# Kernel optimization log

Measured on AMD Instinct MI355X. Metric: run time of the kernel, lower is better.

Reference implementation:

```python
import jax, jax.numpy as jnp
import numpy as np

N_NODES = 50000
N_EDGES = 800000
D = 128


def setup_inputs() -> dict:
    key = jax.random.key(0)
    ks = jax.random.split(key, 7)
    stdv = 1.0 / np.sqrt(D)
    inputs = jax.random.normal(ks[0], (N_NODES, D), dtype=jnp.float32)
    weight = jax.random.uniform(ks[1], (D, D), dtype=jnp.float32, minval=-stdv, maxval=stdv)
    bias = jax.random.uniform(ks[2], (D,), dtype=jnp.float32, minval=-stdv, maxval=stdv)
    alpha = jax.random.uniform(ks[3], (2, 1, 1), dtype=jnp.float32, minval=-3.0, maxval=3.0)
    adj_vals = jax.random.uniform(ks[4], (N_EDGES,), dtype=jnp.float32)
    adj_rows = jax.random.randint(ks[5], (N_EDGES,), 0, N_NODES, dtype=jnp.int32)
    adj_cols = jax.random.randint(ks[6], (N_EDGES,), 0, N_NODES, dtype=jnp.int32)
    return {"inputs": inputs, "weight": weight, "bias": bias, "alpha": alpha,
            "adj_vals": adj_vals, "adj_rows": adj_rows, "adj_cols": adj_cols}


def reference(inputs, weight, bias, alpha, adj_vals, adj_rows, adj_cols):
    n = inputs.shape[0]
    # support = inputs @ weight  (dense GEMM; spmm with dense lhs == matmul)
    support = inputs @ weight                                  # [N, D]
    # output = adj @ support  as COO SpMM: gather source rows, scale, scatter-add
    gathered = support[adj_cols] * adj_vals[:, None]           # [E, D]
    agg = jax.ops.segment_sum(gathered, adj_rows, num_segments=n)  # [N, D]
    # softmax-gated combine of [agg, inputs] (stack order: output first)
    gate = jax.nn.softmax(alpha, axis=0)                       # [2,1,1]
    out = agg * gate[0] + inputs * gate[1]                     # [N, D]
    return jax.nn.elu(out + bias)
```

## Files before the change

kernel.cpp:

```cpp
#include <hip/hip_runtime.h>

#define N_NODES 50000
#define N_EDGES 800000
#define D 128

typedef __attribute__((ext_vector_type(8))) short bf16x8;
typedef __attribute__((ext_vector_type(4))) float f32x4;
typedef __attribute__((ext_vector_type(4))) short short4v;

__device__ __forceinline__ short f2bf(float f) {
    unsigned u = __float_as_uint(f);
    unsigned r = u + 0x7FFFu + ((u >> 16) & 1u);
    return (short)(r >> 16);
}
__device__ __forceinline__ float bf2f(short s) {
    return __uint_as_float(((unsigned)(unsigned short)s) << 16);
}

__global__ __launch_bounds__(256) void gemm_hist_kernel(
    const float* __restrict__ inp, const float* __restrict__ W,
    short* __restrict__ support, const int* __restrict__ rows,
    int* __restrict__ counts, int nGemmBlocks)
{
    if ((int)blockIdx.x >= nGemmBlocks) {
        int e = ((int)blockIdx.x - nGemmBlocks) * 256 + threadIdx.x;
        if (e < N_EDGES) atomicAdd(&counts[rows[e]], 1);
        return;
    }

    __shared__ short Wt[128][136];
    const int tid = threadIdx.x;

    #pragma unroll
    for (int i = 0; i < 16; ++i) {
        int lin = i * 1024 + tid * 4;
        int k = lin >> 7, c = lin & 127;
        float4 w = *(const float4*)&W[lin];
        Wt[c + 0][k] = f2bf(w.x);
        Wt[c + 1][k] = f2bf(w.y);
        Wt[c + 2][k] = f2bf(w.z);
        Wt[c + 3][k] = f2bf(w.w);
    }
    __syncthreads();

    const int wid = tid >> 6, lane = tid & 63;
    const int lr = lane & 15;
    const int lg = lane >> 4;
    const int m0 = (int)blockIdx.x * 64 + wid * 16;

    int arow = m0 + lr;
    if (arow >= N_NODES) arow = 0;
    const float* aptr = &inp[(size_t)arow * D + lg * 8];

    f32x4 acc[8] = {};
    #pragma unroll
    for (int kc = 0; kc < 4; ++kc) {
        float4 a0 = *(const float4*)(aptr + kc * 32);
        float4 a1 = *(const float4*)(aptr + kc * 32 + 4);
        bf16x8 af;
        af[0] = f2bf(a0.x); af[1] = f2bf(a0.y); af[2] = f2bf(a0.z); af[3] = f2bf(a0.w);
        af[4] = f2bf(a1.x); af[5] = f2bf(a1.y); af[6] = f2bf(a1.z); af[7] = f2bf(a1.w);
        #pragma unroll
        for (int t = 0; t < 8; ++t) {
            const bf16x8 bf = *(const bf16x8*)&Wt[t * 16 + lr][kc * 32 + lg * 8];
            acc[t] = __builtin_amdgcn_mfma_f32_16x16x32_bf16(af, bf, acc[t], 0, 0, 0);
        }
    }
    #pragma unroll
    for (int t = 0; t < 8; ++t) {
        #pragma unroll
        for (int r = 0; r < 4; ++r) {
            int orow = m0 + lg * 4 + r;
            if (orow < N_NODES)
                support[(size_t)orow * D + t * 16 + lr] = f2bf(acc[t][r]);
        }
    }
}

__global__ __launch_bounds__(256) void scan_fused(
    const int* __restrict__ counts, int* __restrict__ offsets,
    int* __restrict__ cursor, unsigned long long* __restrict__ aggFlag,
    int* __restrict__ ticket)
{
    __shared__ int s[256];
    __shared__ int bid_s, prefix_s;
    if (threadIdx.x == 0) bid_s = atomicAdd(ticket, 1);
    __syncthreads();
    const int bid = bid_s;
    const int gid = bid * 256 + threadIdx.x;
    int v = (gid < N_NODES) ? counts[gid] : 0;
    s[threadIdx.x] = v;
    __syncthreads();
    #pragma unroll
    for (int d = 1; d < 256; d <<= 1) {
        int t = (threadIdx.x >= d) ? s[threadIdx.x - d] : 0;
        __syncthreads();
        s[threadIdx.x] += t;
        __syncthreads();
    }
    if (threadIdx.x == 0) {
        unsigned long long pk = (1ULL << 63) | (unsigned long long)(unsigned)s[255];
        __hip_atomic_store(&aggFlag[bid], pk, __ATOMIC_RELAXED, __HIP_MEMORY_SCOPE_AGENT);
    }
    if (threadIdx.x < 64) {
        int sum = 0;
        for (int j = threadIdx.x; j < bid; j += 64) {
            unsigned long long pk;
            while (((pk = __hip_atomic_load(&aggFlag[j], __ATOMIC_RELAXED,
                                            __HIP_MEMORY_SCOPE_AGENT)) >> 63) == 0)
                __builtin_amdgcn_s_sleep(1);
            sum += (int)(unsigned)(pk & 0xFFFFFFFFULL);
        }
        #pragma unroll
        for (int d = 1; d < 64; d <<= 1) sum += __shfl_xor(sum, d);
        if (threadIdx.x == 0) prefix_s = sum;
    }
    __syncthreads();
    if (gid < N_NODES) {
        int o = prefix_s + s[threadIdx.x] - v;
        offsets[gid] = o;
        cursor[gid] = o;
    }
    if (gid == 0) offsets[N_NODES] = N_EDGES;
}

#define SCAT_GROUPS 8
#define SCAT_BPG    392
__global__ __launch_bounds__(256) void scatter_kernel(
    const int* __restrict__ rows, const int* __restrict__ cols,
    const float* __restrict__ vals, int* __restrict__ cursor,
    int2* __restrict__ pairs)
{
    const int g  = blockIdx.x & (SCAT_GROUPS - 1);
    const int gi = blockIdx.x >> 3;
    const int rowLo = g * (N_NODES / SCAT_GROUPS);
    const int rowHi = rowLo + (N_NODES / SCAT_GROUPS);

    for (int e = gi * 256 + threadIdx.x; e < N_EDGES; e += SCAT_BPG * 256) {
        int r = rows[e];
        if (r >= rowLo && r < rowHi) {
            int p = atomicAdd(&cursor[r], 1);
            int2 pk;
            pk.x = cols[e];
            pk.y = __float_as_int(vals[e]);
            pairs[p] = pk;
        }
    }
}

__global__ __launch_bounds__(256) void agg_fused(
    const short* __restrict__ support, const int* __restrict__ offsets,
    const int2* __restrict__ pairs,
    const float* __restrict__ inp, const float* __restrict__ bias,
    const float* __restrict__ alpha, float* __restrict__ out)
{
    const int wv = (blockIdx.x * 256 + threadIdx.x) >> 6;
    const int lane = threadIdx.x & 63;
    if (wv >= N_NODES) return;
    const int half = lane >> 5;
    const int li = lane & 31;

    const int start = offsets[wv];
    const int end   = offsets[wv + 1];

    const float4 x = *(const float4*)&inp[(size_t)wv * D + li * 4];
    const float4 b4 = *(const float4*)&bias[li * 4];
    const float a0 = alpha[0], a1 = alpha[1];

    float4 acc = make_float4(0.f, 0.f, 0.f, 0.f);
    int e = start;
    for (; e + 8 <= end; e += 8) {
        int2 p0 = pairs[e + 0 + half];
        int2 p1 = pairs[e + 2 + half];
        int2 p2 = pairs[e + 4 + half];
        int2 p3 = pairs[e + 6 + half];
        short4v s0 = *(const short4v*)&support[(size_t)p0.x * D + li * 4];
        short4v s1 = *(const short4v*)&support[(size_t)p1.x * D + li * 4];
        short4v s2 = *(const short4v*)&support[(size_t)p2.x * D + li * 4];
        short4v s3 = *(const short4v*)&support[(size_t)p3.x * D + li * 4];
        float v0 = __int_as_float(p0.y), v1 = __int_as_float(p1.y);
        float v2 = __int_as_float(p2.y), v3 = __int_as_float(p3.y);
        acc.x += v0 * bf2f(s0[0]) + v1 * bf2f(s1[0]) + v2 * bf2f(s2[0]) + v3 * bf2f(s3[0]);
        acc.y += v0 * bf2f(s0[1]) + v1 * bf2f(s1[1]) + v2 * bf2f(s2[1]) + v3 * bf2f(s3[1]);
        acc.z += v0 * bf2f(s0[2]) + v1 * bf2f(s1[2]) + v2 * bf2f(s2[2]) + v3 * bf2f(s3[2]);
        acc.w += v0 * bf2f(s0[3]) + v1 * bf2f(s1[3]) + v2 * bf2f(s2[3]) + v3 * bf2f(s3[3]);
    }
    for (; e < end; e += 2) {
        int idx = e + half;
        int2 p = (idx < end) ? pairs[idx] : make_int2(0, 0);
        float v = __int_as_float(p.y);
        short4v s = *(const short4v*)&support[(size_t)p.x * D + li * 4];
        acc.x += v * bf2f(s[0]);
        acc.y += v * bf2f(s[1]);
        acc.z += v * bf2f(s[2]);
        acc.w += v * bf2f(s[3]);
    }

    acc.x += __shfl_xor(acc.x, 32);
    acc.y += __shfl_xor(acc.y, 32);
    acc.z += __shfl_xor(acc.z, 32);
    acc.w += __shfl_xor(acc.w, 32);

    const float m = fmaxf(a0, a1);
    const float e0 = __expf(a0 - m), e1 = __expf(a1 - m);
    const float inv = 1.f / (e0 + e1);
    const float g0 = e0 * inv, g1 = e1 * inv;

    float t0 = acc.x * g0 + x.x * g1 + b4.x;
    float t1 = acc.y * g0 + x.y * g1 + b4.y;
    float t2 = acc.z * g0 + x.z * g1 + b4.z;
    float t3 = acc.w * g0 + x.w * g1 + b4.w;
    float r0 = t0 > 0.f ? t0 : (__expf(t0) - 1.f);
    float r1 = t1 > 0.f ? t1 : (__expf(t1) - 1.f);
    float r2 = t2 > 0.f ? t2 : (__expf(t2) - 1.f);
    float r3 = t3 > 0.f ? t3 : (__expf(t3) - 1.f);

    float2 o = (half == 0) ? make_float2(r0, r1) : make_float2(r2, r3);
    *(float2*)&out[(size_t)wv * D + li * 4 + half * 2] = o;
}

extern "C" void kernel_launch(void* const* d_in, const int* in_sizes, int n_in,
                              void* d_out, int out_size, void* d_ws, size_t ws_size,
                              hipStream_t stream)
{
    const float* inp   = (const float*)d_in[0];
    const float* W     = (const float*)d_in[1];
    const float* bias  = (const float*)d_in[2];
    const float* alpha = (const float*)d_in[3];
    const float* vals  = (const float*)d_in[4];
    const int*   rows  = (const int*)d_in[5];
    const int*   cols  = (const int*)d_in[6];
    float* out = (float*)d_out;

    short* support  = (short*)d_ws;
    int*   counts   = (int*)(support + (size_t)N_NODES * D);
    int*   ticket   = counts + N_NODES;
    unsigned long long* aggFlag = (unsigned long long*)(ticket + 2);
    int*   offsets  = (int*)(aggFlag + 256);
    int*   cursor   = offsets + N_NODES + 1;
    int2*  pairs    = (int2*)(cursor + N_NODES + 1);

    const int nGemmBlocks = (N_NODES + 63) / 64;
    const int nEdgeBlocks = (N_EDGES + 255) / 256;
    const int nScanBlocks = (N_NODES + 255) / 256;

    (void)hipMemsetAsync(counts, 0, (size_t)(N_NODES + 2 + 512) * sizeof(int), stream);

    gemm_hist_kernel<<<nGemmBlocks + nEdgeBlocks, 256, 0, stream>>>(
        inp, W, support, rows, counts, nGemmBlocks);
    scan_fused<<<nScanBlocks, 256, 0, stream>>>(counts, offsets, cursor,
                                                aggFlag, ticket);
    scatter_kernel<<<SCAT_GROUPS * SCAT_BPG, 256, 0, stream>>>(
        rows, cols, vals, cursor, pairs);
    agg_fused<<<(N_NODES * 64 + 255) / 256, 256, 0, stream>>>(
        support, offsets, pairs, inp, bias, alpha, out);
}
```

Measured before the change: 206.4 us.

## Pretranspose weight to bf16 once and deepen gather unroll in aggregation

A small prep kernel converts W to a transposed bf16 array in global memory once, so each of the ~780 GEMM blocks no longer converts and transposes W into shared memory. The GEMM reads B fragments straight from global/L2 instead of LDS. The aggregation loop adds a 16-edge unrolled stage that issues 8 independent gathers per lane to raise memory-level parallelism. The trade-offs are an extra kernel launch, more L2 traffic for W fragments and higher register pressure in the aggregation kernel.

```diff
diff --git a/kernel.cpp b/kernel.cpp
--- a/kernel.cpp
+++ b/kernel.cpp
@@ -17,8 +17,31 @@
     return __uint_as_float(((unsigned)(unsigned short)s) << 16);
 }
 
+__global__ __launch_bounds__(256) void prep_w(const float* __restrict__ W,
+                                              short* __restrict__ Wt)
+{
+    __shared__ short Ls[128][17];
+    const int b = blockIdx.x;
+    const int t = threadIdx.x;
+    #pragma unroll
+    for (int i = 0; i < 8; ++i) {
+        int lin = i * 256 + t;
+        int kk = lin >> 7;
+        int c  = lin & 127;
+        Ls[c][kk] = f2bf(W[(b * 16 + kk) * 128 + c]);
+    }
+    __syncthreads();
+    #pragma unroll
+    for (int i = 0; i < 8; ++i) {
+        int lin = i * 256 + t;
+        int c  = lin >> 4;
+        int kk = lin & 15;
+        Wt[c * 128 + b * 16 + kk] = Ls[c][kk];
+    }
+}
+
 __global__ __launch_bounds__(256) void gemm_hist_kernel(
-    const float* __restrict__ inp, const float* __restrict__ W,
+    const float* __restrict__ inp, const short* __restrict__ Wt,
     short* __restrict__ support, const int* __restrict__ rows,
     int* __restrict__ counts, int nGemmBlocks)
 {
@@ -28,21 +51,7 @@
         return;
     }
 
-    __shared__ short Wt[128][136];
     const int tid = threadIdx.x;
-
-    #pragma unroll
-    for (int i = 0; i < 16; ++i) {
-        int lin = i * 1024 + tid * 4;
-        int k = lin >> 7, c = lin & 127;
-        float4 w = *(const float4*)&W[lin];
-        Wt[c + 0][k] = f2bf(w.x);
-        Wt[c + 1][k] = f2bf(w.y);
-        Wt[c + 2][k] = f2bf(w.z);
-        Wt[c + 3][k] = f2bf(w.w);
-    }
-    __syncthreads();
-
     const int wid = tid >> 6, lane = tid & 63;
     const int lr = lane & 15;
     const int lg = lane >> 4;
@@ -62,7 +71,7 @@
         af[4] = f2bf(a1.x); af[5] = f2bf(a1.y); af[6] = f2bf(a1.z); af[7] = f2bf(a1.w);
         #pragma unroll
         for (int t = 0; t < 8; ++t) {
-            const bf16x8 bf = *(const bf16x8*)&Wt[t * 16 + lr][kc * 32 + lg * 8];
+            const bf16x8 bf = *(const bf16x8*)&Wt[(t * 16 + lr) * 128 + kc * 32 + lg * 8];
             acc[t] = __builtin_amdgcn_mfma_f32_16x16x32_bf16(af, bf, acc[t], 0, 0, 0);
         }
     }
@@ -169,6 +178,23 @@
 
     float4 acc = make_float4(0.f, 0.f, 0.f, 0.f);
     int e = start;
+    for (; e + 16 <= end; e += 16) {
+        int2 p[8];
+        #pragma unroll
+        for (int j = 0; j < 8; ++j) p[j] = pairs[e + 2 * j + half];
+        short4v s[8];
+        #pragma unroll
+        for (int j = 0; j < 8; ++j)
+            s[j] = *(const short4v*)&support[(size_t)p[j].x * D + li * 4];
+        #pragma unroll
+        for (int j = 0; j < 8; ++j) {
+            float v = __int_as_float(p[j].y);
+            acc.x += v * bf2f(s[j][0]);
+            acc.y += v * bf2f(s[j][1]);
+            acc.z += v * bf2f(s[j][2]);
+            acc.w += v * bf2f(s[j][3]);
+        }
+    }
     for (; e + 8 <= end; e += 8) {
         int2 p0 = pairs[e + 0 + half];
         int2 p1 = pairs[e + 2 + half];
@@ -233,7 +259,8 @@
     float* out = (float*)d_out;
 
     short* support  = (short*)d_ws;
-    int*   counts   = (int*)(support + (size_t)N_NODES * D);
+    short* Wt       = support + (size_t)N_NODES * D;
+    int*   counts   = (int*)(Wt + 128 * 128);
     int*   ticket   = counts + N_NODES;
     unsigned long long* aggFlag = (unsigned long long*)(ticket + 2);
     int*   offsets  = (int*)(aggFlag + 256);
@@ -246,8 +273,9 @@
 
     (void)hipMemsetAsync(counts, 0, (size_t)(N_NODES + 2 + 512) * sizeof(int), stream);
 
+    prep_w<<<8, 256, 0, stream>>>(W, Wt);
     gemm_hist_kernel<<<nGemmBlocks + nEdgeBlocks, 256, 0, stream>>>(
-        inp, W, support, rows, counts, nGemmBlocks);
+        inp, Wt, support, rows, counts, nGemmBlocks);
     scan_fused<<<nScanBlocks, 256, 0, stream>>>(counts, offsets, cursor,
                                                 aggFlag, ticket);
     scatter_kernel<<<SCAT_GROUPS * SCAT_BPG, 256, 0, stream>>>(
```

After: 214.5 us. 3.9% more time.
